# Kernel tuning notes

Hardware: AMD Instinct MI355X
Metric: run time of the kernel (lower is better)

The kernel has to match this reference:

```python
import jax, jax.numpy as jnp
import numpy as np

B, S, H = 4, 2048, 768
ROUTING_GAIN = 1.0
LN_EPS = 1e-5
MAS_EPS = 1e-9


def _mas_normalize(logits):
    m = jnp.max(jnp.abs(logits), axis=-1, keepdims=True)
    return jax.nn.relu(logits / (m + MAS_EPS))


def _layer_norm(x, w, b):
    mu = jnp.mean(x, axis=-1, keepdims=True)
    var = jnp.var(x, axis=-1, keepdims=True)
    return (x - mu) / jnp.sqrt(var + LN_EPS) * w + b


def _spl(x, proto, gate, mu_w, mu_b):
    # SparseProtoLinear: comp = x @ mu_w.T + mu_b ; match = x @ proto.T / sqrt(d_in) ; gate_logit = x @ gate.T
    scale = 1.0 / jnp.sqrt(jnp.asarray(x.shape[-1], x.dtype))
    match = jnp.einsum('bsd,od->bso', x, proto) * scale
    gate_logit = jnp.einsum('bsd,od->bso', x, gate)
    comp = jnp.einsum('bsd,od->bso', x, mu_w) + mu_b
    return comp, match, gate_logit


def _gate_branch(inp, comp, match, gate_logit):
    routing_logits = (match - _mas_normalize(gate_logit)) * ROUTING_GAIN
    return (inp + comp) * _mas_normalize(routing_logits)


def _rotate_half(x):
    x1, x2 = jnp.split(x, 2, axis=-1)
    return jnp.concatenate([-x2, x1], axis=-1)


def _apply_rope(q, k, cos, sin):
    return q * cos + _rotate_half(q) * sin, k * cos + _rotate_half(k) * sin


def _causal_attention(q, k, v):
    # single-head SDPA over full hidden dim, causal
    d = q.shape[-1]
    scores = jnp.einsum('bqd,bkd->bqk', q, k) / jnp.sqrt(jnp.asarray(d, q.dtype))
    mask = jnp.tril(jnp.ones((q.shape[1], k.shape[1]), dtype=bool))
    scores = jnp.where(mask, scores, jnp.asarray(-jnp.inf, scores.dtype))
    p = jax.nn.softmax(scores, axis=-1)
    return jnp.einsum('bqk,bkd->bqd', p, v)


def setup_inputs() -> dict:
    key = jax.random.key(0)
    ks = iter(jax.random.split(key, 32))
    w_std = 1.0 / np.sqrt(H)
    inp = {'x': jax.random.normal(next(ks), (B, S, H), jnp.float32)}
    # rotary tables: half-dim frequencies duplicated to full hidden dim
    inv_freq = 1.0 / (10000.0 ** (np.arange(0, H, 2, dtype=np.float32) / H))
    ang = np.arange(S, dtype=np.float32)[:, None] * inv_freq[None, :]  # [S, H/2]
    ang = np.concatenate([ang, ang], axis=-1)  # [S, H]
    inp['cos'] = jnp.asarray(np.cos(ang))
    inp['sin'] = jnp.asarray(np.sin(ang))
    inp['ln1_w'] = jnp.ones((H,), jnp.float32)
    inp['ln1_b'] = jnp.zeros((H,), jnp.float32)
    inp['ln2_w'] = jnp.ones((H,), jnp.float32)
    inp['ln2_b'] = jnp.zeros((H,), jnp.float32)
    for name in ['q', 'k', 'v', 'o', 'f1', 'f2']:
        inp[f'{name}_proto'] = jax.random.normal(next(ks), (H, H), jnp.float32) * w_std
        inp[f'{name}_gate'] = jax.random.normal(next(ks), (H, H), jnp.float32) * w_std
        inp[f'{name}_mu_w'] = jax.random.normal(next(ks), (H, H), jnp.float32) * w_std
        inp[f'{name}_mu_b'] = jnp.zeros((H,), jnp.float32)
    return inp


def reference(x, cos, sin, ln1_w, ln1_b, ln2_w, ln2_b,
              q_proto, q_gate, q_mu_w, q_mu_b,
              k_proto, k_gate, k_mu_w, k_mu_b,
              v_proto, v_gate, v_mu_w, v_mu_b,
              o_proto, o_gate, o_mu_w, o_mu_b,
              f1_proto, f1_gate, f1_mu_w, f1_mu_b,
              f2_proto, f2_gate, f2_mu_w, f2_mu_b):
    # prev_protos is None => effective_proto == proto_weight; past_kv is None => causal attention
    ln1_out = _layer_norm(x, ln1_w, ln1_b)
    c_q, mv_q, pc_q = _spl(ln1_out, q_proto, q_gate, q_mu_w, q_mu_b)
    c_k, mv_k, pc_k = _spl(ln1_out, k_proto, k_gate, k_mu_w, k_mu_b)
    c_v, mv_v, pc_v = _spl(ln1_out, v_proto, v_gate, v_mu_w, v_mu_b)
    q = _gate_branch(ln1_out, c_q, mv_q, pc_q)
    k = _gate_branch(ln1_out, c_k, mv_k, pc_k)
    v = _gate_branch(ln1_out, c_v, mv_v, pc_v)
    q, k = _apply_rope(q, k, cos, sin)
    attn_out = _causal_attention(q, k, v)
    c_o, mv_o, pc_o = _spl(attn_out, o_proto, o_gate, o_mu_w, o_mu_b)
    m_o = _gate_branch(attn_out, c_o, mv_o, pc_o)
    x = x + m_o
    ln2_out = _layer_norm(x, ln2_w, ln2_b)
    c1, mv1, pc1 = _spl(ln2_out, f1_proto, f1_gate, f1_mu_w, f1_mu_b)
    h_act = jax.nn.relu(_gate_branch(ln2_out, c1, mv1, pc1))
    c2, mv2, pc2 = _spl(h_act, f2_proto, f2_gate, f2_mu_w, f2_mu_b)
    m2 = _gate_branch(h_act, c2, mv2, pc2)
    x_out = x + m2
    return x_out
```

## Files before the change

### kernel.cpp

```cpp
#include <hip/hip_runtime.h>
#include <hip/hip_bf16.h>
#include <math.h>

#define B_ 4
#define S_ 2048
#define H_ 768
#define M_ (B_*S_)
#define MN ((size_t)M_*(size_t)H_)
#define HH (H_*H_)
#define SS ((size_t)S_*(size_t)S_)
#define SH ((size_t)S_*(size_t)H_)
#define NQKV 6912
#define N3   2304

typedef __bf16 bf16_t;
typedef __bf16 bf16x8 __attribute__((ext_vector_type(8)));
typedef __bf16 bf16x4 __attribute__((ext_vector_type(4)));
typedef float  f32x4  __attribute__((ext_vector_type(4)));
typedef unsigned short u16;
typedef u16 u16x4 __attribute__((ext_vector_type(4)));

typedef __attribute__((address_space(3))) void       lds_void_t;
typedef __attribute__((address_space(1))) const void gvoid_t;

__device__ __forceinline__ float b2f(u16 u){ unsigned x = (unsigned)u << 16; float f; __builtin_memcpy(&f,&x,4); return f; }
__device__ __forceinline__ u16 f2b(float f){ bf16_t h = (bf16_t)f; u16 u; __builtin_memcpy(&u,&h,2); return u; }

template<bool MAXOP>
__device__ __forceinline__ float blockReduce(float v, float* s){
  #pragma unroll
  for (int o = 32; o; o >>= 1){
    float t = __shfl_xor(v, o);
    v = MAXOP ? fmaxf(v, t) : (v + t);
  }
  int lane = threadIdx.x & 63, w = threadIdx.x >> 6;
  if (lane == 0) s[w] = v;
  __syncthreads();
  float r = s[0];
  #pragma unroll
  for (int i = 1; i < 4; i++) r = MAXOP ? fmaxf(r, s[i]) : (r + s[i]);
  __syncthreads();
  return r;
}

__device__ __forceinline__ float waveMax(float v){
  #pragma unroll
  for (int o = 1; o < 64; o <<= 1) v = fmaxf(v, __shfl_xor(v, o));
  return v;
}
__device__ __forceinline__ float waveSum(float v){
  #pragma unroll
  for (int o = 1; o < 64; o <<= 1) v += __shfl_xor(v, o);
  return v;
}

struct W18 { const float* p[18]; };

__global__ __launch_bounds__(256) void conv_weights(W18 w, bf16_t* __restrict__ out, float rs){
  int m = blockIdx.y;
  float sc = (m % 3 == 1) ? rs : 1.0f;
  int i = (blockIdx.x * 256 + threadIdx.x) * 4;
  f32x4 v = *(const f32x4*)(w.p[m] + i);
  bf16x4 o; o[0]=(bf16_t)(v[0]*sc); o[1]=(bf16_t)(v[1]*sc); o[2]=(bf16_t)(v[2]*sc); o[3]=(bf16_t)(v[3]*sc);
  *(bf16x4*)(out + (size_t)m * HH + i) = o;
}

__global__ __launch_bounds__(256) void ln_kernel(const float* __restrict__ x,
                                                 const float* __restrict__ w,
                                                 const float* __restrict__ b,
                                                 bf16_t* __restrict__ outb){
  int wid = threadIdx.x >> 6, l = threadIdx.x & 63;
  int row = blockIdx.x * 4 + wid;
  size_t base = (size_t)row * H_ + l*12;
  float v[12];
  #pragma unroll
  for (int i = 0; i < 3; i++){
    f32x4 t = *(const f32x4*)(x + base + 4*i);
    #pragma unroll
    for (int j = 0; j < 4; j++) v[4*i+j] = t[j];
  }
  float s1 = 0.f, s2 = 0.f;
  #pragma unroll
  for (int j = 0; j < 12; j++){ s1 += v[j]; s2 += v[j]*v[j]; }
  s1 = waveSum(s1); s2 = waveSum(s2);
  float mu = s1 * (1.f/H_), var = s2 * (1.f/H_) - mu*mu;
  float rstd = rsqrtf(var + 1e-5f);
  #pragma unroll
  for (int i = 0; i < 3; i++){
    f32x4 wv = *(const f32x4*)(w + l*12 + 4*i);
    f32x4 bv = *(const f32x4*)(b + l*12 + 4*i);
    u16x4 u;
    #pragma unroll
    for (int j = 0; j < 4; j++) u[j] = f2b((v[4*i+j]-mu)*rstd*wv[j] + bv[j]);
    *(u16x4*)(outb + base + 4*i) = u;
  }
}

__global__ __launch_bounds__(256) void gemm_bt(const bf16_t* __restrict__ A,
                                               const bf16_t* __restrict__ Bm,
                                               bf16_t* __restrict__ C,
                                               int M, int N, int K,
                                               long sA, long sB, long sC, int cmode){
  __shared__ bf16_t As[3][128*32];
  __shared__ bf16_t Bs[3][128*32];

  int gx = gridDim.x, gy = gridDim.y;
  int nwg = gx * gy * gridDim.z;
  int id  = (blockIdx.z * gy + blockIdx.y) * gx + blockIdx.x;
  int cpx = nwg >> 3;
  int nrb = cpx / gx;
  int x   = id & 7;
  int local = id >> 3;
  int bx  = local / nrb;
  int frow = x * nrb + (local % nrb);
  int by  = frow % gy;
  int z   = frow / gy;

  A  += (size_t)z * sA;
  Bm += (size_t)z * sB;
  C  += (size_t)z * sC;

  int row0 = by * 128, col0 = bx * 128;
  if (cmode == 1 && col0 > row0) return;

  int tid  = threadIdx.x;
  int lane = tid & 63;
  int wave = tid >> 6;
  int wm = wave >> 1, wn = wave & 1;
  int lr = lane & 15, kg = lane >> 4;

  f32x4 acc[4][4] = {};
  int NT = K >> 5;
  if (cmode == 2) { int lim = (row0 + 128) >> 5; NT = NT < lim ? NT : lim; }

  auto stage = [&](int buf, int kt){
    int kk = kt * 32;
    #pragma unroll
    for (int i = 0; i < 2; i++){
      int c  = tid + i*256;
      int r  = c >> 2;
      int scol = ((c & 3) ^ ((r >> 1) & 3)) * 8;
      __builtin_amdgcn_global_load_lds((gvoid_t*)(A  + (size_t)(row0 + r)*K + kk + scol),
                                       (lds_void_t*)(&As[buf][c*8]), 16, 0, 0);
      __builtin_amdgcn_global_load_lds((gvoid_t*)(Bm + (size_t)(col0 + r)*K + kk + scol),
                                       (lds_void_t*)(&Bs[buf][c*8]), 16, 0, 0);
    }
  };

  stage(0, 0);
  stage(1, 1);
  asm volatile("s_waitcnt vmcnt(4)" ::: "memory");
  __builtin_amdgcn_s_barrier();
  __builtin_amdgcn_sched_barrier(0);

  int b0 = 0, b1 = 1, b2 = 2;
  for (int kt = 0; kt < NT; ++kt){
    if (kt + 2 < NT) stage(b2, kt + 2);
    bf16x8 af[4], bfr[4];
    #pragma unroll
    for (int m = 0; m < 4; m++){
      int r = wm*64 + m*16 + lr;
      af[m] = *reinterpret_cast<const bf16x8*>(&As[b0][r*32 + ((kg ^ ((r >> 1) & 3)) * 8)]);
    }
    #pragma unroll
    for (int n = 0; n < 4; n++){
      int r = wn*64 + n*16 + lr;
      bfr[n] = *reinterpret_cast<const bf16x8*>(&Bs[b0][r*32 + ((kg ^ ((r >> 1) & 3)) * 8)]);
    }
    #pragma unroll
    for (int m = 0; m < 4; m++)
      #pragma unroll
      for (int n = 0; n < 4; n++)
        acc[m][n] = __builtin_amdgcn_mfma_f32_16x16x32_bf16(af[m], bfr[n], acc[m][n], 0, 0, 0);
    if (kt + 1 < NT){
      if (kt + 2 < NT) asm volatile("s_waitcnt vmcnt(4)" ::: "memory");
      else             asm volatile("s_waitcnt vmcnt(0)" ::: "memory");
      __builtin_amdgcn_s_barrier();
      __builtin_amdgcn_sched_barrier(0);
    }
    int tmp = b0; b0 = b1; b1 = b2; b2 = tmp;
  }

  #pragma unroll
  for (int m = 0; m < 4; m++){
    int rb = row0 + wm*64 + m*16 + kg*4;
    #pragma unroll
    for (int n = 0; n < 4; n++){
      int cc = col0 + wn*64 + n*16 + lr;
      #pragma unroll
      for (int r = 0; r < 4; r++)
        C[(size_t)(rb + r)*N + cc] = (bf16_t)acc[m][n][r];
    }
  }
}

__global__ __launch_bounds__(256) void gate_kernel(const bf16_t* __restrict__ inp,
                                                   const bf16_t* __restrict__ c3,
                                                   long ldc, int colbase,
                                                   const float* __restrict__ bias,
                                                   const float* __restrict__ cosT,
                                                   const float* __restrict__ sinT,
                                                   const float* __restrict__ resid,
                                                   const float* __restrict__ lnw,
                                                   const float* __restrict__ lnb,
                                                   float* __restrict__ outf,
                                                   bf16_t* __restrict__ outb,
                                                   float oscale, int mode){
  int wid = threadIdx.x >> 6, l = threadIdx.x & 63;
  int row = blockIdx.x * 4 + wid;
  size_t bi = (size_t)row * H_ + l*12;
  size_t bc = (size_t)row * ldc + colbase + l*12;

  float iv[12], cv[12], mv[12], gv[12];
  float gmax = 0.f;
  #pragma unroll
  for (int i = 0; i < 3; i++){
    u16x4 a = *(const u16x4*)(inp + bi + 4*i);
    u16x4 b = *(const u16x4*)(c3 + bc + 4*i);
    u16x4 c = *(const u16x4*)(c3 + bc + 768 + 4*i);
    u16x4 d = *(const u16x4*)(c3 + bc + 1536 + 4*i);
    f32x4 bv = *(const f32x4*)(bias + l*12 + 4*i);
    #pragma unroll
    for (int j = 0; j < 4; j++){
      iv[4*i+j] = b2f(a[j]); cv[4*i+j] = b2f(b[j]) + bv[j];
      mv[4*i+j] = b2f(c[j]); gv[4*i+j] = b2f(d[j]);
      gmax = fmaxf(gmax, fabsf(gv[4*i+j]));
    }
  }
  gmax = waveMax(gmax);
  float rg = 1.f / (gmax + 1e-9f);

  float rt[12], rmax = 0.f;
  #pragma unroll
  for (int j = 0; j < 12; j++){
    rt[j] = mv[j] - fmaxf(gv[j]*rg, 0.f);
    rmax  = fmaxf(rmax, fabsf(rt[j]));
  }
  rmax = waveMax(rmax);
  float rr = 1.f / (rmax + 1e-9f);

  float val[12];
  #pragma unroll
  for (int j = 0; j < 12; j++) val[j] = (iv[j] + cv[j]) * fmaxf(rt[j]*rr, 0.f) * oscale;

  if (mode == 0){
    int s = row & (S_ - 1);
    const float* cp = cosT + (size_t)s*H_ + l*12;
    const float* sp = sinT + (size_t)s*H_ + l*12;
    #pragma unroll
    for (int i = 0; i < 3; i++){
      f32x4 cw = *(const f32x4*)(cp + 4*i);
      f32x4 sw = *(const f32x4*)(sp + 4*i);
      u16x4 u;
      #pragma unroll
      for (int j = 0; j < 4; j++){
        int q = 4*i + j;
        float partner = __shfl_xor(val[q], 32);
        if (l < 32) partner = -partner;
        u[j] = f2b(val[q]*cw[j] + partner*sw[j]);
      }
      *(u16x4*)(outb + bi + 4*i) = u;
    }
  } else if (mode == 1 || mode == 3){
    #pragma unroll
    for (int i = 0; i < 3; i++){
      u16x4 u;
      #pragma unroll
      for (int j = 0; j < 4; j++){
        float v = val[4*i+j];
        if (mode == 3) v = fmaxf(v, 0.f);
        u[j] = f2b(v);
      }
      *(u16x4*)(outb + bi + 4*i) = u;
    }
  } else if (mode == 2){
    #pragma unroll
    for (int i = 0; i < 3; i++){
      f32x4 rv = *(const f32x4*)(resid + bi + 4*i);
      f32x4 ov;
      #pragma unroll
      for (int j = 0; j < 4; j++) ov[j] = val[4*i+j] + rv[j];
      *(f32x4*)(outf + bi + 4*i) = ov;
    }
  } else {
    float xv[12];
    #pragma unroll
    for (int i = 0; i < 3; i++){
      f32x4 rv = *(const f32x4*)(resid + bi + 4*i);
      f32x4 ov;
      #pragma unroll
      for (int j = 0; j < 4; j++){ xv[4*i+j] = val[4*i+j] + rv[j]; ov[j] = xv[4*i+j]; }
      *(f32x4*)(outf + bi + 4*i) = ov;
    }
    float s1 = 0.f, s2 = 0.f;
    #pragma unroll
    for (int j = 0; j < 12; j++){ s1 += xv[j]; s2 += xv[j]*xv[j]; }
    s1 = waveSum(s1); s2 = waveSum(s2);
    float mu = s1 * (1.f/H_), var = s2 * (1.f/H_) - mu*mu;
    float rstd = rsqrtf(var + 1e-5f);
    #pragma unroll
    for (int i = 0; i < 3; i++){
      f32x4 wv = *(const f32x4*)(lnw + l*12 + 4*i);
      f32x4 bv = *(const f32x4*)(lnb + l*12 + 4*i);
      u16x4 u;
      #pragma unroll
      for (int j = 0; j < 4; j++) u[j] = f2b((xv[4*i+j]-mu)*rstd*wv[j] + bv[j]);
      *(u16x4*)(outb + bi + 4*i) = u;
    }
  }
}

__global__ __launch_bounds__(256) void softmax_causal(const bf16_t* __restrict__ sc,
                                                      bf16_t* __restrict__ P){
  __shared__ float red[4];
  int r = blockIdx.x, b = blockIdx.y, t = threadIdx.x;
  const bf16_t* srow = sc + (size_t)b*SS + (size_t)r * S_;
  bf16_t* prow = P + (size_t)b*SS + (size_t)r * S_;
  int n = r + 1;
  int fill = ((r >> 7) + 1) << 7;
  float m = -1e30f;
  for (int j = t; j < n; j += 256) m = fmaxf(m, (float)srow[j]);
  m = blockReduce<true>(m, red);
  float sum = 0.f;
  for (int j = t; j < n; j += 256) sum += __expf((float)srow[j] - m);
  sum = blockReduce<false>(sum, red);
  float inv = 1.f / sum;
  for (int j = t; j < fill; j += 256)
    prow[j] = (j < n) ? (bf16_t)(__expf((float)srow[j] - m)*inv) : (bf16_t)0.f;
}

__global__ __launch_bounds__(256) void transpose_bf(const bf16_t* __restrict__ in,
                                                    bf16_t* __restrict__ out){
  __shared__ bf16_t tile[32][33];
  int bz = blockIdx.z;
  const bf16_t* I = in  + (size_t)bz * SH;
  bf16_t*       O = out + (size_t)bz * SH;
  int s0 = blockIdx.x*32, h0 = blockIdx.y*32;
  int tx = threadIdx.x, ty = threadIdx.y;
  #pragma unroll
  for (int k = 0; k < 4; k++)
    tile[ty + 8*k][tx] = I[(size_t)(s0 + ty + 8*k)*H_ + h0 + tx];
  __syncthreads();
  #pragma unroll
  for (int k = 0; k < 4; k++)
    O[(size_t)(h0 + ty + 8*k)*S_ + s0 + tx] = tile[tx][ty + 8*k];
}

extern "C" void kernel_launch(void* const* d_in, const int* in_sizes, int n_in,
                              void* d_out, int out_size, void* d_ws, size_t ws_size,
                              hipStream_t stream){
  const float* x    = (const float*)d_in[0];
  const float* cosT = (const float*)d_in[1];
  const float* sinT = (const float*)d_in[2];
  const float* ln1w = (const float*)d_in[3];
  const float* ln1b = (const float*)d_in[4];
  const float* ln2w = (const float*)d_in[5];
  const float* ln2b = (const float*)d_in[6];

  W18 wp; const float* bias[6];
  for (int i = 0; i < 6; i++){
    const float* proto = (const float*)d_in[7 + 4*i + 0];
    const float* gatep = (const float*)d_in[7 + 4*i + 1];
    const float* muw   = (const float*)d_in[7 + 4*i + 2];
    bias[i]            = (const float*)d_in[7 + 4*i + 3];
    wp.p[i*3 + 0] = muw;
    wp.p[i*3 + 1] = proto;
    wp.p[i*3 + 2] = gatep;
  }

  char* w = (char*)d_ws;
  auto alloc = [&](size_t bytes){ void* r = (void*)w; w += (bytes + 255) & ~(size_t)255; return r; };
  bf16_t* w_bf   = (bf16_t*)alloc((size_t)18 * HH * 2);
  bf16_t* a_bf   = (bf16_t*)alloc(MN * 2);
  bf16_t* h_bf   = (bf16_t*)alloc(MN * 2);
  bf16_t* c3b    = (bf16_t*)alloc((size_t)M_ * NQKV * 2);
  bf16_t* q_bf   = (bf16_t*)alloc(MN * 2);
  bf16_t* k_bf   = (bf16_t*)alloc(MN * 2);
  bf16_t* v_bf   = (bf16_t*)alloc(MN * 2);
  bf16_t* vt     = (bf16_t*)alloc(MN * 2);
  bf16_t* attn_b = (bf16_t*)alloc(MN * 2);
  float*  x1     = (float*) alloc(MN * 4);
  (void)ws_size;
  bf16_t* sc_bf = c3b;
  bf16_t* p_bf  = c3b + B_ * SS;

  const float rs = 1.0f / sqrtf((float)H_);

  conv_weights<<<dim3(HH/1024, 18), 256, 0, stream>>>(wp, w_bf, rs);
  ln_kernel<<<M_/4, 256, 0, stream>>>(x, ln1w, ln1b, a_bf);

  gemm_bt<<<dim3(NQKV/128, M_/128, 1), 256, 0, stream>>>(
      a_bf, w_bf, c3b, M_, NQKV, H_, 0, 0, 0, 0);
  gate_kernel<<<M_/4, 256, 0, stream>>>(a_bf, c3b, NQKV, 0,    bias[0], cosT, sinT, nullptr, nullptr, nullptr, nullptr, q_bf, rs,  0);
  gate_kernel<<<M_/4, 256, 0, stream>>>(a_bf, c3b, NQKV, 2304, bias[1], cosT, sinT, nullptr, nullptr, nullptr, nullptr, k_bf, 1.f, 0);
  gate_kernel<<<M_/4, 256, 0, stream>>>(a_bf, c3b, NQKV, 4608, bias[2], nullptr, nullptr, nullptr, nullptr, nullptr, nullptr, v_bf, 1.f, 1);

  transpose_bf<<<dim3(S_/32, H_/32, B_), dim3(32, 8), 0, stream>>>(v_bf, vt);

  gemm_bt<<<dim3(S_/128, S_/128, B_), 256, 0, stream>>>(
      q_bf, k_bf, sc_bf, S_, S_, H_, (long)SH, (long)SH, (long)SS, 1);

  softmax_causal<<<dim3(S_, B_), 256, 0, stream>>>(sc_bf, p_bf);

  gemm_bt<<<dim3(H_/128, S_/128, B_), 256, 0, stream>>>(
      p_bf, vt, attn_b, S_, H_, S_, (long)SS, (long)SH, (long)SH, 2);

  gemm_bt<<<dim3(N3/128, M_/128, 1), 256, 0, stream>>>(
      attn_b, w_bf + (size_t)9*HH, c3b, M_, N3, H_, 0, 0, 0, 0);
  gate_kernel<<<M_/4, 256, 0, stream>>>(attn_b, c3b, N3, 0, bias[3], nullptr, nullptr, x, ln2w, ln2b, x1, a_bf, 1.f, 4);

  gemm_bt<<<dim3(N3/128, M_/128, 1), 256, 0, stream>>>(
      a_bf, w_bf + (size_t)12*HH, c3b, M_, N3, H_, 0, 0, 0, 0);
  gate_kernel<<<M_/4, 256, 0, stream>>>(a_bf, c3b, N3, 0, bias[4], nullptr, nullptr, nullptr, nullptr, nullptr, nullptr, h_bf, 1.f, 3);

  gemm_bt<<<dim3(N3/128, M_/128, 1), 256, 0, stream>>>(
      h_bf, w_bf + (size_t)15*HH, c3b, M_, N3, H_, 0, 0, 0, 0);
  gate_kernel<<<M_/4, 256, 0, stream>>>(h_bf, c3b, N3, 0, bias[5], nullptr, nullptr, x1, nullptr, nullptr, (float*)d_out, nullptr, 1.f, 2);
}
```

Measured before the change: 470.6 us.

## Double-buffer GEMM with occupancy hint, fuse QKV gates, vectorize causal softmax

The GEMM drops from a three-stage to a two-stage LDS pipeline and adds a minimum-occupancy launch bound of 5, trading prefetch depth for more resident workgroups and less LDS per block. The three separate q/k/v gate launches become one kernel that loads the input row and the RoPE tables once. The causal softmax now keeps one 8-wide vector per thread in registers, so the scores are read once and exp is computed once instead of twice. The shallower pipeline may expose more global-load latency, and the launch bound may force register spills.

```diff
diff --git a/kernel.cpp b/kernel.cpp
--- a/kernel.cpp
+++ b/kernel.cpp
@@ -19,6 +19,7 @@
 typedef float  f32x4  __attribute__((ext_vector_type(4)));
 typedef unsigned short u16;
 typedef u16 u16x4 __attribute__((ext_vector_type(4)));
+typedef u16 u16x8 __attribute__((ext_vector_type(8)));
 
 typedef __attribute__((address_space(3))) void       lds_void_t;
 typedef __attribute__((address_space(1))) const void gvoid_t;
@@ -96,13 +97,13 @@
   }
 }
 
-__global__ __launch_bounds__(256) void gemm_bt(const bf16_t* __restrict__ A,
-                                               const bf16_t* __restrict__ Bm,
-                                               bf16_t* __restrict__ C,
-                                               int M, int N, int K,
-                                               long sA, long sB, long sC, int cmode){
-  __shared__ bf16_t As[3][128*32];
-  __shared__ bf16_t Bs[3][128*32];
+__global__ __launch_bounds__(256, 5) void gemm_bt(const bf16_t* __restrict__ A,
+                                                  const bf16_t* __restrict__ Bm,
+                                                  bf16_t* __restrict__ C,
+                                                  int M, int N, int K,
+                                                  long sA, long sB, long sC, int cmode){
+  __shared__ bf16_t As[2][128*32];
+  __shared__ bf16_t Bs[2][128*32];
 
   int gx = gridDim.x, gy = gridDim.y;
   int nwg = gx * gy * gridDim.z;
@@ -148,37 +149,31 @@
   };
 
   stage(0, 0);
-  stage(1, 1);
-  asm volatile("s_waitcnt vmcnt(4)" ::: "memory");
+  asm volatile("s_waitcnt vmcnt(0)" ::: "memory");
   __builtin_amdgcn_s_barrier();
-  __builtin_amdgcn_sched_barrier(0);
-
-  int b0 = 0, b1 = 1, b2 = 2;
+
+  int buf = 0;
   for (int kt = 0; kt < NT; ++kt){
-    if (kt + 2 < NT) stage(b2, kt + 2);
+    if (kt + 1 < NT) stage(buf ^ 1, kt + 1);
     bf16x8 af[4], bfr[4];
     #pragma unroll
     for (int m = 0; m < 4; m++){
       int r = wm*64 + m*16 + lr;
-      af[m] = *reinterpret_cast<const bf16x8*>(&As[b0][r*32 + ((kg ^ ((r >> 1) & 3)) * 8)]);
+      af[m] = *reinterpret_cast<const bf16x8*>(&As[buf][r*32 + ((kg ^ ((r >> 1) & 3)) * 8)]);
     }
     #pragma unroll
     for (int n = 0; n < 4; n++){
       int r = wn*64 + n*16 + lr;
-      bfr[n] = *reinterpret_cast<const bf16x8*>(&Bs[b0][r*32 + ((kg ^ ((r >> 1) & 3)) * 8)]);
+      bfr[n] = *reinterpret_cast<const bf16x8*>(&Bs[buf][r*32 + ((kg ^ ((r >> 1) & 3)) * 8)]);
     }
     #pragma unroll
     for (int m = 0; m < 4; m++)
       #pragma unroll
       for (int n = 0; n < 4; n++)
         acc[m][n] = __builtin_amdgcn_mfma_f32_16x16x32_bf16(af[m], bfr[n], acc[m][n], 0, 0, 0);
-    if (kt + 1 < NT){
-      if (kt + 2 < NT) asm volatile("s_waitcnt vmcnt(4)" ::: "memory");
-      else             asm volatile("s_waitcnt vmcnt(0)" ::: "memory");
-      __builtin_amdgcn_s_barrier();
-      __builtin_amdgcn_sched_barrier(0);
-    }
-    int tmp = b0; b0 = b1; b1 = b2; b2 = tmp;
+    if (kt + 1 < NT) asm volatile("s_waitcnt vmcnt(0)" ::: "memory");
+    __builtin_amdgcn_s_barrier();
+    buf ^= 1;
   }
 
   #pragma unroll
@@ -190,6 +185,99 @@
       #pragma unroll
       for (int r = 0; r < 4; r++)
         C[(size_t)(rb + r)*N + cc] = (bf16_t)acc[m][n][r];
+    }
+  }
+}
+
+__global__ __launch_bounds__(256) void gate_qkv(const bf16_t* __restrict__ inp,
+                                                const bf16_t* __restrict__ c3,
+                                                const float* __restrict__ b_q,
+                                                const float* __restrict__ b_k,
+                                                const float* __restrict__ b_v,
+                                                const float* __restrict__ cosT,
+                                                const float* __restrict__ sinT,
+                                                bf16_t* __restrict__ q_o,
+                                                bf16_t* __restrict__ k_o,
+                                                bf16_t* __restrict__ v_o,
+                                                float rs){
+  int wid = threadIdx.x >> 6, l = threadIdx.x & 63;
+  int row = blockIdx.x * 4 + wid;
+  size_t bi = (size_t)row * H_ + l*12;
+  size_t brow = (size_t)row * NQKV + l*12;
+
+  float iv[12];
+  #pragma unroll
+  for (int i = 0; i < 3; i++){
+    u16x4 a = *(const u16x4*)(inp + bi + 4*i);
+    #pragma unroll
+    for (int j = 0; j < 4; j++) iv[4*i+j] = b2f(a[j]);
+  }
+  int s = row & (S_ - 1);
+  f32x4 cw[3], sw[3];
+  #pragma unroll
+  for (int i = 0; i < 3; i++){
+    cw[i] = *(const f32x4*)(cosT + (size_t)s*H_ + l*12 + 4*i);
+    sw[i] = *(const f32x4*)(sinT + (size_t)s*H_ + l*12 + 4*i);
+  }
+
+  const float* biasp[3] = {b_q, b_k, b_v};
+  bf16_t* outp[3] = {q_o, k_o, v_o};
+
+  #pragma unroll
+  for (int sec = 0; sec < 3; sec++){
+    size_t bc = brow + (size_t)sec * 2304;
+    float cv[12], mv[12], gv[12];
+    float gmax = 0.f;
+    #pragma unroll
+    for (int i = 0; i < 3; i++){
+      u16x4 b = *(const u16x4*)(c3 + bc + 4*i);
+      u16x4 c = *(const u16x4*)(c3 + bc + 768 + 4*i);
+      u16x4 d = *(const u16x4*)(c3 + bc + 1536 + 4*i);
+      f32x4 bv = *(const f32x4*)(biasp[sec] + l*12 + 4*i);
+      #pragma unroll
+      for (int j = 0; j < 4; j++){
+        cv[4*i+j] = b2f(b[j]) + bv[j];
+        mv[4*i+j] = b2f(c[j]);
+        gv[4*i+j] = b2f(d[j]);
+        gmax = fmaxf(gmax, fabsf(gv[4*i+j]));
+      }
+    }
+    gmax = waveMax(gmax);
+    float rg = 1.f / (gmax + 1e-9f);
+    float rt[12], rmax = 0.f;
+    #pragma unroll
+    for (int j = 0; j < 12; j++){
+      rt[j] = mv[j] - fmaxf(gv[j]*rg, 0.f);
+      rmax  = fmaxf(rmax, fabsf(rt[j]));
+    }
+    rmax = waveMax(rmax);
+    float rr = 1.f / (rmax + 1e-9f);
+    float oscale = (sec == 0) ? rs : 1.0f;
+    float val[12];
+    #pragma unroll
+    for (int j = 0; j < 12; j++) val[j] = (iv[j] + cv[j]) * fmaxf(rt[j]*rr, 0.f) * oscale;
+
+    if (sec < 2){
+      #pragma unroll
+      for (int i = 0; i < 3; i++){
+        u16x4 u;
+        #pragma unroll
+        for (int j = 0; j < 4; j++){
+          int q = 4*i + j;
+          float partner = __shfl_xor(val[q], 32);
+          if (l < 32) partner = -partner;
+          u[j] = f2b(val[q]*cw[i][j] + partner*sw[i][j]);
+        }
+        *(u16x4*)(outp[sec] + bi + 4*i) = u;
+      }
+    } else {
+      #pragma unroll
+      for (int i = 0; i < 3; i++){
+        u16x4 u;
+        #pragma unroll
+        for (int j = 0; j < 4; j++) u[j] = f2b(val[4*i+j]);
+        *(u16x4*)(outp[sec] + bi + 4*i) = u;
+      }
     }
   }
 }
@@ -198,14 +286,12 @@
                                                    const bf16_t* __restrict__ c3,
                                                    long ldc, int colbase,
                                                    const float* __restrict__ bias,
-                                                   const float* __restrict__ cosT,
-                                                   const float* __restrict__ sinT,
                                                    const float* __restrict__ resid,
                                                    const float* __restrict__ lnw,
                                                    const float* __restrict__ lnb,
                                                    float* __restrict__ outf,
                                                    bf16_t* __restrict__ outb,
-                                                   float oscale, int mode){
+                                                   int mode){
   int wid = threadIdx.x >> 6, l = threadIdx.x & 63;
   int row = blockIdx.x * 4 + wid;
   size_t bi = (size_t)row * H_ + l*12;
@@ -241,36 +327,14 @@
 
   float val[12];
   #pragma unroll
-  for (int j = 0; j < 12; j++) val[j] = (iv[j] + cv[j]) * fmaxf(rt[j]*rr, 0.f) * oscale;
-
-  if (mode == 0){
-    int s = row & (S_ - 1);
-    const float* cp = cosT + (size_t)s*H_ + l*12;
-    const float* sp = sinT + (size_t)s*H_ + l*12;
-    #pragma unroll
-    for (int i = 0; i < 3; i++){
-      f32x4 cw = *(const f32x4*)(cp + 4*i);
-      f32x4 sw = *(const f32x4*)(sp + 4*i);
-      u16x4 u;
-      #pragma unroll
-      for (int j = 0; j < 4; j++){
-        int q = 4*i + j;
-        float partner = __shfl_xor(val[q], 32);
-        if (l < 32) partner = -partner;
-        u[j] = f2b(val[q]*cw[j] + partner*sw[j]);
-      }
-      *(u16x4*)(outb + bi + 4*i) = u;
-    }
-  } else if (mode == 1 || mode == 3){
+  for (int j = 0; j < 12; j++) val[j] = (iv[j] + cv[j]) * fmaxf(rt[j]*rr, 0.f);
+
+  if (mode == 3){
     #pragma unroll
     for (int i = 0; i < 3; i++){
       u16x4 u;
       #pragma unroll
-      for (int j = 0; j < 4; j++){
-        float v = val[4*i+j];
-        if (mode == 3) v = fmaxf(v, 0.f);
-        u[j] = f2b(v);
-      }
+      for (int j = 0; j < 4; j++) u[j] = f2b(fmaxf(val[4*i+j], 0.f));
       *(u16x4*)(outb + bi + 4*i) = u;
     }
   } else if (mode == 2){
@@ -318,15 +382,36 @@
   bf16_t* prow = P + (size_t)b*SS + (size_t)r * S_;
   int n = r + 1;
   int fill = ((r >> 7) + 1) << 7;
+  int c0 = t * 8;
+
+  float v[8];
   float m = -1e30f;
-  for (int j = t; j < n; j += 256) m = fmaxf(m, (float)srow[j]);
+  if (c0 < n){
+    u16x8 u = *(const u16x8*)(srow + c0);
+    #pragma unroll
+    for (int j = 0; j < 8; j++){
+      v[j] = (c0 + j < n) ? b2f(u[j]) : -1e30f;
+      m = fmaxf(m, v[j]);
+    }
+  } else {
+    #pragma unroll
+    for (int j = 0; j < 8; j++) v[j] = -1e30f;
+  }
   m = blockReduce<true>(m, red);
   float sum = 0.f;
-  for (int j = t; j < n; j += 256) sum += __expf((float)srow[j] - m);
+  #pragma unroll
+  for (int j = 0; j < 8; j++){
+    v[j] = (v[j] > -1e29f) ? __expf(v[j] - m) : 0.f;
+    sum += v[j];
+  }
   sum = blockReduce<false>(sum, red);
   float inv = 1.f / sum;
-  for (int j = t; j < fill; j += 256)
-    prow[j] = (j < n) ? (bf16_t)(__expf((float)srow[j] - m)*inv) : (bf16_t)0.f;
+  if (c0 < fill){
+    u16x8 u;
+    #pragma unroll
+    for (int j = 0; j < 8; j++) u[j] = f2b(v[j] * inv);
+    *(u16x8*)(prow + c0) = u;
+  }
 }
 
 __global__ __launch_bounds__(256) void transpose_bf(const bf16_t* __restrict__ in,
@@ -391,9 +476,8 @@
 
   gemm_bt<<<dim3(NQKV/128, M_/128, 1), 256, 0, stream>>>(
       a_bf, w_bf, c3b, M_, NQKV, H_, 0, 0, 0, 0);
-  gate_kernel<<<M_/4, 256, 0, stream>>>(a_bf, c3b, NQKV, 0,    bias[0], cosT, sinT, nullptr, nullptr, nullptr, nullptr, q_bf, rs,  0);
-  gate_kernel<<<M_/4, 256, 0, stream>>>(a_bf, c3b, NQKV, 2304, bias[1], cosT, sinT, nullptr, nullptr, nullptr, nullptr, k_bf, 1.f, 0);
-  gate_kernel<<<M_/4, 256, 0, stream>>>(a_bf, c3b, NQKV, 4608, bias[2], nullptr, nullptr, nullptr, nullptr, nullptr, nullptr, v_bf, 1.f, 1);
+  gate_qkv<<<M_/4, 256, 0, stream>>>(a_bf, c3b, bias[0], bias[1], bias[2],
+                                     cosT, sinT, q_bf, k_bf, v_bf, rs);
 
   transpose_bf<<<dim3(S_/32, H_/32, B_), dim3(32, 8), 0, stream>>>(v_bf, vt);
 
@@ -407,13 +491,13 @@
 
   gemm_bt<<<dim3(N3/128, M_/128, 1), 256, 0, stream>>>(
       attn_b, w_bf + (size_t)9*HH, c3b, M_, N3, H_, 0, 0, 0, 0);
-  gate_kernel<<<M_/4, 256, 0, stream>>>(attn_b, c3b, N3, 0, bias[3], nullptr, nullptr, x, ln2w, ln2b, x1, a_bf, 1.f, 4);
+  gate_kernel<<<M_/4, 256, 0, stream>>>(attn_b, c3b, N3, 0, bias[3], x, ln2w, ln2b, x1, a_bf, 4);
 
   gemm_bt<<<dim3(N3/128, M_/128, 1), 256, 0, stream>>>(
       a_bf, w_bf + (size_t)12*HH, c3b, M_, N3, H_, 0, 0, 0, 0);
-  gate_kernel<<<M_/4, 256, 0, stream>>>(a_bf, c3b, N3, 0, bias[4], nullptr, nullptr, nullptr, nullptr, nullptr, nullptr, h_bf, 1.f, 3);
+  gate_kernel<<<M_/4, 256, 0, stream>>>(a_bf, c3b, N3, 0, bias[4], nullptr, nullptr, nullptr, nullptr, h_bf, 3);
 
   gemm_bt<<<dim3(N3/128, M_/128, 1), 256, 0, stream>>>(
       h_bf, w_bf + (size_t)15*HH, c3b, M_, N3, H_, 0, 0, 0, 0);
-  gate_kernel<<<M_/4, 256, 0, stream>>>(h_bf, c3b, N3, 0, bias[5], nullptr, nullptr, x1, nullptr, nullptr, (float*)d_out, nullptr, 1.f, 2);
-}
+  gate_kernel<<<M_/4, 256, 0, stream>>>(h_bf, c3b, N3, 0, bias[5], x1, nullptr, nullptr, (float*)d_out, nullptr, 2);
+}
```

Result: slower. 494.3 us (+5.0%).
